# Kernel optimization log

Measured on AMD Instinct MI355X. Metric: run time of the kernel, lower is better.

## Reference

```python
import jax, jax.numpy as jnp
import numpy as np

B, T, J = 64, 1024, 22
PARENTS = [0, 0, 1, 2, 3, 0, 5, 6, 7, 0, 9, 10, 11, 12, 11, 14, 15, 16, 11, 18, 19, 20]
SPARSE_JOINTS = [0, 4, 8, 13, 17, 21]
EE = tuple(SPARSE_JOINTS[1:])                       # end effectors (sparse_joints[1:])
NO_SPARSE = tuple(j for j in range(J) if j not in SPARSE_JOINTS)
LAMBDA_EE, LAMBDA_EE_REG = 1.0, 0.1
IDENT_DQ = np.array([1, 0, 0, 0, 0, 0, 0, 0], dtype=np.float32)


def _qconj(q):
    return q * jnp.array([1.0, -1.0, -1.0, -1.0], q.dtype)


def _qmul(a, b):
    aw, ax, ay, az = a[..., 0], a[..., 1], a[..., 2], a[..., 3]
    bw, bx, by, bz = b[..., 0], b[..., 1], b[..., 2], b[..., 3]
    return jnp.stack([
        aw * bw - ax * bx - ay * by - az * bz,
        aw * bx + ax * bw + ay * bz - az * by,
        aw * by - ax * bz + ay * bw + az * bx,
        aw * bz + ax * by - ay * bx + az * bw], axis=-1)


def _qrot(q, v):
    # rotate vector v by unit quaternion q
    qv = q[..., 1:]
    t = 2.0 * jnp.cross(qv, v)
    return v + q[..., :1] * t + jnp.cross(qv, t)


def _qmat(q):
    w, x, y, z = q[..., 0], q[..., 1], q[..., 2], q[..., 3]
    m = jnp.stack([
        1 - 2 * (y * y + z * z), 2 * (x * y - w * z), 2 * (x * z + w * y),
        2 * (x * y + w * z), 1 - 2 * (x * x + z * z), 2 * (y * z - w * x),
        2 * (x * z - w * y), 2 * (y * z + w * x), 1 - 2 * (x * x + y * y)], axis=-1)
    return m.reshape(m.shape[:-1] + (3, 3))


def _denorm_to_dq(x, mean, std, set_root_identity):
    # x: (B, J*8, T) channel-major dual quats -> (B, T, J, 8)
    x = x * std[None, :, None] + mean[None, :, None]
    if set_root_identity:
        x = x.at[:, :8, :].set(jnp.asarray(IDENT_DQ, x.dtype)[None, :, None])
    b, c, t = x.shape
    return x.reshape(b, c // 8, 8, t).transpose(0, 3, 1, 2)


def _local_rot_from_dq(dq):
    # skeleton_from_dual_quat: real part = global rotation; make local via parent gather
    qr = dq[..., :4]
    qr = qr / jnp.linalg.norm(qr, axis=-1, keepdims=True)
    parent = jnp.asarray(PARENTS)
    local = _qmul(_qconj(qr[:, :, parent, :]), qr)   # (B,T,J,4)
    # forward_ik overwrites root local rotation with identity
    local = local.at[:, :, 0, :].set(jnp.array([1.0, 0.0, 0.0, 0.0], dq.dtype))
    return local


def _fk(local_rot, offsets):
    # fk_2: sequential parent-indexed propagation; root global pos is zeros
    rots = [local_rot[:, :, 0]]
    poss = [jnp.zeros(local_rot.shape[:2] + (3,), local_rot.dtype)]
    for j in range(1, J):
        p = PARENTS[j]
        rots.append(_qmul(rots[p], local_rot[:, :, j]))
        poss.append(_qrot(rots[p], offsets[j]) + poss[p])
    grot = jnp.stack(rots, axis=2)          # (B,T,J,4)
    pos = jnp.stack(poss, axis=2)           # (B,T,J,3)
    return pos, _qmat(grot)                  # positions, (B,T,J,3,3) rot matrices


def setup_inputs() -> dict:
    key = jax.random.key(0)
    ks = jax.random.split(key, 7)
    C = J * 8
    return {
        "input": jax.random.normal(ks[0], (B, C, T), jnp.float32),
        "input_ik": jax.random.normal(ks[1], (B, C - 8, T), jnp.float32),
        "input_decoder": jax.random.normal(ks[2], (B, C, T), jnp.float32),
        "target": jax.random.normal(ks[3], (B, C, T), jnp.float32),
        "mean_dqs": 0.1 * jax.random.normal(ks[4], (C,), jnp.float32),
        "std_dqs": 0.5 + 0.5 * jax.random.uniform(ks[5], (C,), jnp.float32),
        "offsets": jax.random.normal(ks[6], (J, 3), jnp.float32),
    }


def reference(input, input_ik, input_decoder, target, mean_dqs, std_dqs, offsets):
    # prepend identity-slot for the root (8 zero channels), then denormalize
    dq_ik = jnp.concatenate([jnp.zeros_like(input_ik[:, :8, :]), input_ik], axis=1)
    dq_ik = _denorm_to_dq(dq_ik, mean_dqs, std_dqs, True)
    dq_dec = _denorm_to_dq(input_decoder, mean_dqs, std_dqs, True)
    dq_tgt = _denorm_to_dq(target, mean_dqs, std_dqs, False)

    r_ik = _local_rot_from_dq(dq_ik)
    r_dec = _local_rot_from_dq(dq_dec)
    r_tgt = _local_rot_from_dq(dq_tgt)

    pos, rm = _fk(r_ik, offsets)
    tpos, trm = _fk(r_tgt, offsets)
    dpos, drm = _fk(r_dec, offsets)

    ee = jnp.asarray(EE)
    ns = jnp.asarray(NO_SPARSE)
    mse = lambda a, b: jnp.mean((a - b) ** 2)
    loss_ee = mse(pos[:, :, ee], tpos[:, :, ee]) + mse(rm[:, :, ee], trm[:, :, ee])
    loss_reg = mse(dpos[:, :, ns], pos[:, :, ns]) + mse(drm[:, :, ns], rm[:, :, ns])
    return loss_ee * LAMBDA_EE + loss_reg * LAMBDA_EE_REG
```

## Files before the change

kernel.cpp:

```cpp
#include <hip/hip_runtime.h>


#define T_DIM 1024

struct Q { float w, x, y, z; };
struct V3 { float x, y, z; };
struct St { Q rot; V3 pos; };

__device__ __forceinline__ Q qmul(const Q a, const Q b) {
    Q r;
    r.w = a.w*b.w - a.x*b.x - a.y*b.y - a.z*b.z;
    r.x = a.w*b.x + a.x*b.w + a.y*b.z - a.z*b.y;
    r.y = a.w*b.y - a.x*b.z + a.y*b.w + a.z*b.x;
    r.z = a.w*b.z + a.x*b.y - a.y*b.x + a.z*b.w;
    return r;
}

__device__ __forceinline__ V3 qrot(const Q q, const V3 v) {
    float tx = 2.f*(q.y*v.z - q.z*v.y);
    float ty = 2.f*(q.z*v.x - q.x*v.z);
    float tz = 2.f*(q.x*v.y - q.y*v.x);
    V3 r;
    r.x = v.x + q.w*tx + (q.y*tz - q.z*ty);
    r.y = v.y + q.w*ty + (q.z*tx - q.x*tz);
    r.z = v.z + q.w*tz + (q.x*ty - q.y*tx);
    return r;
}

__device__ __forceinline__ float rmdiff2u(const Q a, const Q b) {
    float d = a.w*b.w + a.x*b.x + a.y*b.y + a.z*b.z;
    return 8.f*(1.f - d*d);
}

__device__ __forceinline__ float pdiff2(const V3 a, const V3 b) {
    float dx=a.x-b.x, dy=a.y-b.y, dz=a.z-b.z;
    return dx*dx+dy*dy+dz*dz;
}

__device__ __forceinline__ V3 v3add(const V3 a, const V3 b) {
    return V3{a.x+b.x, a.y+b.y, a.z+b.z};
}

__device__ __forceinline__ Q mkq(const float r[4], const int c0,
                                 const float* __restrict__ mean,
                                 const float* __restrict__ stdv) {
    Q q;
    q.w = r[0]*stdv[c0+0] + mean[c0+0];
    q.x = r[1]*stdv[c0+1] + mean[c0+1];
    q.y = r[2]*stdv[c0+2] + mean[c0+2];
    q.z = r[3]*stdv[c0+3] + mean[c0+3];
    float inv = rsqrtf(q.w*q.w + q.x*q.x + q.y*q.y + q.z*q.z);
    q.w*=inv; q.x*=inv; q.y*=inv; q.z*=inv;
    return q;
}

template<int J0, int N>
__device__ __forceinline__ void pf2(
    const float* __restrict__ xp, const float* __restrict__ yp,
    float (*xr)[4], float (*yr)[4])
{
#pragma unroll
    for (int jj = 0; jj < N; ++jj) {
        const int j = J0 + jj;
#pragma unroll
        for (int c = 0; c < 4; ++c) {
            xr[jj][c] = xp[(j*8 + c)*T_DIM];
            yr[jj][c] = yp[(j*8 + c)*T_DIM];
        }
    }
}

template<int J, bool LOSS, bool PRE>
__device__ __forceinline__ void step2(
    St& sx, St& sy,
    const float xr[4], const float yr[4],
    const float* __restrict__ mean, const float* __restrict__ stdv,
    const float* __restrict__ offs, const Q q0c,
    float& ap, float& ar)
{
    const int c0 = J*8;
    Q qx = mkq(xr, c0, mean, stdv);
    Q qy = mkq(yr, c0, mean, stdv);
    if (PRE) qy = qmul(q0c, qy);
    V3 off = { offs[3*J], offs[3*J+1], offs[3*J+2] };
    V3 px = v3add(qrot(sx.rot, off), sx.pos);
    V3 py = v3add(qrot(sy.rot, off), sy.pos);
    if (LOSS) {
        ap += pdiff2(px, py);
        ar += rmdiff2u(qx, qy);
    }
    sx.rot = qx; sx.pos = px;
    sy.rot = qy; sy.pos = py;
}

template<bool EEROLE>
__device__ __forceinline__ void walk(
    const float* __restrict__ xp, const float* __restrict__ yp,
    const float* __restrict__ mean, const float* __restrict__ stdv,
    const float* __restrict__ offs,
    float& ap, float& ar)
{
    float Xa[4][4], Ya[4][4];
    float Xb[4][4], Yb[4][4];
    float Xc[5][4], Yc[5][4];
    float Xd[4][4], Yd[4][4];
    float Xe[4][4], Ye[4][4];
    float rq0[4];

    if (EEROLE) {
#pragma unroll
        for (int c = 0; c < 4; ++c) rq0[c] = yp[c*T_DIM];
    }
    pf2<1,4>(xp, yp, Xa, Ya);
    pf2<5,4>(xp, yp, Xb, Yb);

    Q q0c = {1.f, 0.f, 0.f, 0.f};
    if (EEROLE) {
        Q q0 = mkq(rq0, 0, mean, stdv);
        q0c = { q0.w, -q0.x, -q0.y, -q0.z };
    }
    const St root = { {1.f,0.f,0.f,0.f}, {0.f,0.f,0.f} };
    St sx, sy;

    sx = root; sy = root;
    step2<1, !EEROLE, EEROLE>(sx,sy, Xa[0],Ya[0], mean,stdv,offs,q0c, ap,ar);
    step2<2, !EEROLE, EEROLE>(sx,sy, Xa[1],Ya[1], mean,stdv,offs,q0c, ap,ar);
    step2<3, !EEROLE, EEROLE>(sx,sy, Xa[2],Ya[2], mean,stdv,offs,q0c, ap,ar);
    step2<4,  EEROLE, EEROLE>(sx,sy, Xa[3],Ya[3], mean,stdv,offs,q0c, ap,ar);

    pf2<9,5>(xp, yp, Xc, Yc);

    sx = root; sy = root;
    step2<5, !EEROLE, EEROLE>(sx,sy, Xb[0],Yb[0], mean,stdv,offs,q0c, ap,ar);
    step2<6, !EEROLE, EEROLE>(sx,sy, Xb[1],Yb[1], mean,stdv,offs,q0c, ap,ar);
    step2<7, !EEROLE, EEROLE>(sx,sy, Xb[2],Yb[2], mean,stdv,offs,q0c, ap,ar);
    step2<8,  EEROLE, EEROLE>(sx,sy, Xb[3],Yb[3], mean,stdv,offs,q0c, ap,ar);

    pf2<14,4>(xp, yp, Xd, Yd);

    sx = root; sy = root;
    step2<9,  !EEROLE, EEROLE>(sx,sy, Xc[0],Yc[0], mean,stdv,offs,q0c, ap,ar);
    step2<10, !EEROLE, EEROLE>(sx,sy, Xc[1],Yc[1], mean,stdv,offs,q0c, ap,ar);
    step2<11, !EEROLE, EEROLE>(sx,sy, Xc[2],Yc[2], mean,stdv,offs,q0c, ap,ar);
    const St sx11 = sx, sy11 = sy;
    step2<12, !EEROLE, EEROLE>(sx,sy, Xc[3],Yc[3], mean,stdv,offs,q0c, ap,ar);
    step2<13,  EEROLE, EEROLE>(sx,sy, Xc[4],Yc[4], mean,stdv,offs,q0c, ap,ar);

    pf2<18,4>(xp, yp, Xe, Ye);

    sx = sx11; sy = sy11;
    step2<14, !EEROLE, EEROLE>(sx,sy, Xd[0],Yd[0], mean,stdv,offs,q0c, ap,ar);
    step2<15, !EEROLE, EEROLE>(sx,sy, Xd[1],Yd[1], mean,stdv,offs,q0c, ap,ar);
    step2<16, !EEROLE, EEROLE>(sx,sy, Xd[2],Yd[2], mean,stdv,offs,q0c, ap,ar);
    step2<17,  EEROLE, EEROLE>(sx,sy, Xd[3],Yd[3], mean,stdv,offs,q0c, ap,ar);

    sx = sx11; sy = sy11;
    step2<18, !EEROLE, EEROLE>(sx,sy, Xe[0],Ye[0], mean,stdv,offs,q0c, ap,ar);
    step2<19, !EEROLE, EEROLE>(sx,sy, Xe[1],Ye[1], mean,stdv,offs,q0c, ap,ar);
    step2<20, !EEROLE, EEROLE>(sx,sy, Xe[2],Ye[2], mean,stdv,offs,q0c, ap,ar);
    step2<21,  EEROLE, EEROLE>(sx,sy, Xe[3],Ye[3], mean,stdv,offs,q0c, ap,ar);
}

__global__ __launch_bounds__(256, 2) void fk_loss_kernel(
    const float* __restrict__ ik, const float* __restrict__ dec,
    const float* __restrict__ tgt, const float* __restrict__ mean,
    const float* __restrict__ stdv, const float* __restrict__ offs,
    float* __restrict__ out)
{
    __shared__ float swred[4];
    const int tid = threadIdx.x;
    const int bid = blockIdx.x;
    const int role = bid >> 8;
    const int pose_blk = bid & 255;

    const int p = pose_blk * 256 + tid;
    const int b = p >> 10;
    const int t = p & 1023;
    const float* ikp = ik  + (size_t)b * (168*1024) + t - (size_t)(8*T_DIM);
    const float* dep = dec + (size_t)b * (176*1024) + t;
    const float* tgp = tgt + (size_t)b * (176*1024) + t;

    float ap = 0.f, ar = 0.f;
    float loss;
    const float BT = 65536.f;
    if (role == 0) {
        walk<true>(ikp, tgp, mean, stdv, offs, ap, ar);
        loss = ap * (1.0f/(BT*15.f)) + ar * (1.0f/(BT*45.f));
    } else {
        walk<false>(dep, ikp, mean, stdv, offs, ap, ar);
        loss = ap * (0.1f/(BT*48.f)) + ar * (0.1f/(BT*144.f));
    }

#pragma unroll
    for (int o = 32; o > 0; o >>= 1) loss += __shfl_down(loss, o);
    if ((tid & 63) == 0) swred[tid >> 6] = loss;
    __syncthreads();
    if (tid == 0) {
        atomicAdd(out, swred[0]+swred[1]+swred[2]+swred[3]);
    }
}

extern "C" void kernel_launch(void* const* d_in, const int* in_sizes, int n_in,
                              void* d_out, int out_size, void* d_ws, size_t ws_size,
                              hipStream_t stream) {
    const float* ikx  = (const float*)d_in[1];
    const float* dec  = (const float*)d_in[2];
    const float* tgt  = (const float*)d_in[3];
    const float* mean = (const float*)d_in[4];
    const float* stdv = (const float*)d_in[5];
    const float* offs = (const float*)d_in[6];
    float* out = (float*)d_out;

    hipMemsetAsync(out, 0, sizeof(float), stream);
    fk_loss_kernel<<<512, 256, 0, stream>>>(ikx, dec, tgt, mean, stdv, offs, out);
}
```

Before: 195.4 us.

## Process two timesteps per thread with float2 loads and packed math

Each thread now handles two adjacent timesteps using 8-byte float2 loads and paired arithmetic that can map to packed FP32 instructions. The grid is halved to 256 blocks. The prefetch plan changes from deep whole-chain register buffers to a smaller reused buffer loaded in pieces, and the occupancy hint in launch bounds is dropped. This aims to improve load width and ALU throughput, but it halves the number of threads, which lowers latency hiding for a memory-bound kernel and leaves most CUs partly idle.

```diff
diff --git a/kernel.cpp b/kernel.cpp
--- a/kernel.cpp
+++ b/kernel.cpp
@@ -3,12 +3,23 @@
 
 #define T_DIM 1024
 
-struct Q { float w, x, y, z; };
-struct V3 { float x, y, z; };
-struct St { Q rot; V3 pos; };
-
-__device__ __forceinline__ Q qmul(const Q a, const Q b) {
-    Q r;
+struct alignas(8) F2 { float u, v; };
+
+__device__ __forceinline__ F2 operator+(F2 a, F2 b){ return {a.u+b.u, a.v+b.v}; }
+__device__ __forceinline__ F2 operator-(F2 a, F2 b){ return {a.u-b.u, a.v-b.v}; }
+__device__ __forceinline__ F2 operator*(F2 a, F2 b){ return {a.u*b.u, a.v*b.v}; }
+__device__ __forceinline__ F2 operator*(F2 a, float s){ return {a.u*s, a.v*s}; }
+__device__ __forceinline__ F2 operator+(F2 a, float s){ return {a.u+s, a.v+s}; }
+__device__ __forceinline__ F2 f2neg(F2 a){ return {-a.u, -a.v}; }
+__device__ __forceinline__ F2 f2bc(float s){ return {s, s}; }
+__device__ __forceinline__ F2 f2rsq(F2 a){ return {rsqrtf(a.u), rsqrtf(a.v)}; }
+
+struct Q2 { F2 w, x, y, z; };
+struct V2 { F2 x, y, z; };
+struct St2 { Q2 rot; V2 pos; };
+
+__device__ __forceinline__ Q2 qmul2(const Q2 a, const Q2 b) {
+    Q2 r;
     r.w = a.w*b.w - a.x*b.x - a.y*b.y - a.z*b.z;
     r.x = a.w*b.x + a.x*b.w + a.y*b.z - a.z*b.y;
     r.y = a.w*b.y - a.x*b.z + a.y*b.w + a.z*b.x;
@@ -16,78 +27,79 @@
     return r;
 }
 
-__device__ __forceinline__ V3 qrot(const Q q, const V3 v) {
-    float tx = 2.f*(q.y*v.z - q.z*v.y);
-    float ty = 2.f*(q.z*v.x - q.x*v.z);
-    float tz = 2.f*(q.x*v.y - q.y*v.x);
-    V3 r;
-    r.x = v.x + q.w*tx + (q.y*tz - q.z*ty);
-    r.y = v.y + q.w*ty + (q.z*tx - q.x*tz);
-    r.z = v.z + q.w*tz + (q.x*ty - q.y*tx);
+__device__ __forceinline__ V2 qrot2(const Q2 q, float ox, float oy, float oz) {
+    F2 tx = (q.y*oz - q.z*oy)*2.f;
+    F2 ty = (q.z*ox - q.x*oz)*2.f;
+    F2 tz = (q.x*oy - q.y*ox)*2.f;
+    V2 r;
+    r.x = (q.w*tx + (q.y*tz - q.z*ty)) + ox;
+    r.y = (q.w*ty + (q.z*tx - q.x*tz)) + oy;
+    r.z = (q.w*tz + (q.x*ty - q.y*tx)) + oz;
     return r;
 }
 
-__device__ __forceinline__ float rmdiff2u(const Q a, const Q b) {
-    float d = a.w*b.w + a.x*b.x + a.y*b.y + a.z*b.z;
-    return 8.f*(1.f - d*d);
-}
-
-__device__ __forceinline__ float pdiff2(const V3 a, const V3 b) {
-    float dx=a.x-b.x, dy=a.y-b.y, dz=a.z-b.z;
-    return dx*dx+dy*dy+dz*dz;
-}
-
-__device__ __forceinline__ V3 v3add(const V3 a, const V3 b) {
-    return V3{a.x+b.x, a.y+b.y, a.z+b.z};
-}
-
-__device__ __forceinline__ Q mkq(const float r[4], const int c0,
-                                 const float* __restrict__ mean,
-                                 const float* __restrict__ stdv) {
-    Q q;
+__device__ __forceinline__ F2 rmdiff2u(const Q2 a, const Q2 b) {
+    F2 d = a.w*b.w + a.x*b.x + a.y*b.y + a.z*b.z;
+    return (f2bc(1.f) - d*d)*8.f;
+}
+
+__device__ __forceinline__ F2 pdiff2(const V2 a, const V2 b) {
+    F2 dx = a.x-b.x, dy = a.y-b.y, dz = a.z-b.z;
+    return dx*dx + dy*dy + dz*dz;
+}
+
+__device__ __forceinline__ Q2 mkq2(const F2 r[4], const int c0,
+                                   const float* __restrict__ mean,
+                                   const float* __restrict__ stdv) {
+    Q2 q;
     q.w = r[0]*stdv[c0+0] + mean[c0+0];
     q.x = r[1]*stdv[c0+1] + mean[c0+1];
     q.y = r[2]*stdv[c0+2] + mean[c0+2];
     q.z = r[3]*stdv[c0+3] + mean[c0+3];
-    float inv = rsqrtf(q.w*q.w + q.x*q.x + q.y*q.y + q.z*q.z);
-    q.w*=inv; q.x*=inv; q.y*=inv; q.z*=inv;
+    F2 inv = f2rsq(q.w*q.w + q.x*q.x + q.y*q.y + q.z*q.z);
+    q.w = q.w*inv; q.x = q.x*inv; q.y = q.y*inv; q.z = q.z*inv;
     return q;
 }
 
+__device__ __forceinline__ F2 ld2(const float* __restrict__ base, int idx) {
+    return *reinterpret_cast<const F2*>(base + idx);
+}
+
 template<int J0, int N>
-__device__ __forceinline__ void pf2(
-    const float* __restrict__ xp, const float* __restrict__ yp,
-    float (*xr)[4], float (*yr)[4])
+__device__ __forceinline__ void ldb(
+    const float* __restrict__ xp, const float* __restrict__ yp, const int t0,
+    F2 (*X)[4], F2 (*Y)[4])
 {
 #pragma unroll
     for (int jj = 0; jj < N; ++jj) {
-        const int j = J0 + jj;
 #pragma unroll
         for (int c = 0; c < 4; ++c) {
-            xr[jj][c] = xp[(j*8 + c)*T_DIM];
-            yr[jj][c] = yp[(j*8 + c)*T_DIM];
+            X[jj][c] = ld2(xp, ((J0+jj)*8 + c)*T_DIM + t0);
+            Y[jj][c] = ld2(yp, ((J0+jj)*8 + c)*T_DIM + t0);
         }
     }
 }
 
 template<int J, bool LOSS, bool PRE>
-__device__ __forceinline__ void step2(
-    St& sx, St& sy,
-    const float xr[4], const float yr[4],
+__device__ __forceinline__ void stepf(
+    St2& sx, St2& sy,
+    const F2 xr[4], const F2 yr[4],
     const float* __restrict__ mean, const float* __restrict__ stdv,
-    const float* __restrict__ offs, const Q q0c,
-    float& ap, float& ar)
+    const float* __restrict__ offs, const Q2& q0c,
+    F2& ap, F2& ar)
 {
     const int c0 = J*8;
-    Q qx = mkq(xr, c0, mean, stdv);
-    Q qy = mkq(yr, c0, mean, stdv);
-    if (PRE) qy = qmul(q0c, qy);
-    V3 off = { offs[3*J], offs[3*J+1], offs[3*J+2] };
-    V3 px = v3add(qrot(sx.rot, off), sx.pos);
-    V3 py = v3add(qrot(sy.rot, off), sy.pos);
+    Q2 qx = mkq2(xr, c0, mean, stdv);
+    Q2 qy = mkq2(yr, c0, mean, stdv);
+    if (PRE) qy = qmul2(q0c, qy);
+    const float ox = offs[3*J], oy = offs[3*J+1], oz = offs[3*J+2];
+    V2 dx = qrot2(sx.rot, ox, oy, oz);
+    V2 dy = qrot2(sy.rot, ox, oy, oz);
+    V2 px = { dx.x + sx.pos.x, dx.y + sx.pos.y, dx.z + sx.pos.z };
+    V2 py = { dy.x + sy.pos.x, dy.y + sy.pos.y, dy.z + sy.pos.z };
     if (LOSS) {
-        ap += pdiff2(px, py);
-        ar += rmdiff2u(qx, qy);
+        ap = ap + pdiff2(px, py);
+        ar = ar + rmdiff2u(qx, qy);
     }
     sx.rot = qx; sx.pos = px;
     sy.rot = qy; sy.pos = py;
@@ -95,73 +107,69 @@
 
 template<bool EEROLE>
 __device__ __forceinline__ void walk(
-    const float* __restrict__ xp, const float* __restrict__ yp,
+    const float* __restrict__ xp, const float* __restrict__ yp, const int t0,
     const float* __restrict__ mean, const float* __restrict__ stdv,
-    const float* __restrict__ offs,
-    float& ap, float& ar)
-{
-    float Xa[4][4], Ya[4][4];
-    float Xb[4][4], Yb[4][4];
-    float Xc[5][4], Yc[5][4];
-    float Xd[4][4], Yd[4][4];
-    float Xe[4][4], Ye[4][4];
-    float rq0[4];
+    const float* __restrict__ offs, F2& ap, F2& ar)
+{
+    F2 X[4][4], Y[4][4];
+    F2 rq0[4];
 
     if (EEROLE) {
 #pragma unroll
-        for (int c = 0; c < 4; ++c) rq0[c] = yp[c*T_DIM];
-    }
-    pf2<1,4>(xp, yp, Xa, Ya);
-    pf2<5,4>(xp, yp, Xb, Yb);
-
-    Q q0c = {1.f, 0.f, 0.f, 0.f};
+        for (int c = 0; c < 4; ++c) rq0[c] = ld2(yp, c*T_DIM + t0);
+    }
+    ldb<1,4>(xp, yp, t0, X, Y);
+
+    Q2 q0c = { f2bc(1.f), f2bc(0.f), f2bc(0.f), f2bc(0.f) };
     if (EEROLE) {
-        Q q0 = mkq(rq0, 0, mean, stdv);
-        q0c = { q0.w, -q0.x, -q0.y, -q0.z };
-    }
-    const St root = { {1.f,0.f,0.f,0.f}, {0.f,0.f,0.f} };
-    St sx, sy;
+        Q2 q0 = mkq2(rq0, 0, mean, stdv);
+        q0c = { q0.w, f2neg(q0.x), f2neg(q0.y), f2neg(q0.z) };
+    }
+    const St2 root = { { f2bc(1.f), f2bc(0.f), f2bc(0.f), f2bc(0.f) },
+                       { f2bc(0.f), f2bc(0.f), f2bc(0.f) } };
+    St2 sx, sy;
 
     sx = root; sy = root;
-    step2<1, !EEROLE, EEROLE>(sx,sy, Xa[0],Ya[0], mean,stdv,offs,q0c, ap,ar);
-    step2<2, !EEROLE, EEROLE>(sx,sy, Xa[1],Ya[1], mean,stdv,offs,q0c, ap,ar);
-    step2<3, !EEROLE, EEROLE>(sx,sy, Xa[2],Ya[2], mean,stdv,offs,q0c, ap,ar);
-    step2<4,  EEROLE, EEROLE>(sx,sy, Xa[3],Ya[3], mean,stdv,offs,q0c, ap,ar);
-
-    pf2<9,5>(xp, yp, Xc, Yc);
-
+    stepf<1, !EEROLE, EEROLE>(sx,sy, X[0],Y[0], mean,stdv,offs,q0c, ap,ar);
+    stepf<2, !EEROLE, EEROLE>(sx,sy, X[1],Y[1], mean,stdv,offs,q0c, ap,ar);
+    stepf<3, !EEROLE, EEROLE>(sx,sy, X[2],Y[2], mean,stdv,offs,q0c, ap,ar);
+    stepf<4,  EEROLE, EEROLE>(sx,sy, X[3],Y[3], mean,stdv,offs,q0c, ap,ar);
+
+    ldb<5,4>(xp, yp, t0, X, Y);
     sx = root; sy = root;
-    step2<5, !EEROLE, EEROLE>(sx,sy, Xb[0],Yb[0], mean,stdv,offs,q0c, ap,ar);
-    step2<6, !EEROLE, EEROLE>(sx,sy, Xb[1],Yb[1], mean,stdv,offs,q0c, ap,ar);
-    step2<7, !EEROLE, EEROLE>(sx,sy, Xb[2],Yb[2], mean,stdv,offs,q0c, ap,ar);
-    step2<8,  EEROLE, EEROLE>(sx,sy, Xb[3],Yb[3], mean,stdv,offs,q0c, ap,ar);
-
-    pf2<14,4>(xp, yp, Xd, Yd);
-
+    stepf<5, !EEROLE, EEROLE>(sx,sy, X[0],Y[0], mean,stdv,offs,q0c, ap,ar);
+    stepf<6, !EEROLE, EEROLE>(sx,sy, X[1],Y[1], mean,stdv,offs,q0c, ap,ar);
+    stepf<7, !EEROLE, EEROLE>(sx,sy, X[2],Y[2], mean,stdv,offs,q0c, ap,ar);
+    stepf<8,  EEROLE, EEROLE>(sx,sy, X[3],Y[3], mean,stdv,offs,q0c, ap,ar);
+
+    ldb<9,3>(xp, yp, t0, X, Y);
     sx = root; sy = root;
-    step2<9,  !EEROLE, EEROLE>(sx,sy, Xc[0],Yc[0], mean,stdv,offs,q0c, ap,ar);
-    step2<10, !EEROLE, EEROLE>(sx,sy, Xc[1],Yc[1], mean,stdv,offs,q0c, ap,ar);
-    step2<11, !EEROLE, EEROLE>(sx,sy, Xc[2],Yc[2], mean,stdv,offs,q0c, ap,ar);
-    const St sx11 = sx, sy11 = sy;
-    step2<12, !EEROLE, EEROLE>(sx,sy, Xc[3],Yc[3], mean,stdv,offs,q0c, ap,ar);
-    step2<13,  EEROLE, EEROLE>(sx,sy, Xc[4],Yc[4], mean,stdv,offs,q0c, ap,ar);
-
-    pf2<18,4>(xp, yp, Xe, Ye);
-
+    stepf<9,  !EEROLE, EEROLE>(sx,sy, X[0],Y[0], mean,stdv,offs,q0c, ap,ar);
+    stepf<10, !EEROLE, EEROLE>(sx,sy, X[1],Y[1], mean,stdv,offs,q0c, ap,ar);
+    stepf<11, !EEROLE, EEROLE>(sx,sy, X[2],Y[2], mean,stdv,offs,q0c, ap,ar);
+    const St2 sx11 = sx, sy11 = sy;
+    ldb<12,2>(xp, yp, t0, X, Y);
+    stepf<12, !EEROLE, EEROLE>(sx,sy, X[0],Y[0], mean,stdv,offs,q0c, ap,ar);
+    stepf<13,  EEROLE, EEROLE>(sx,sy, X[1],Y[1], mean,stdv,offs,q0c, ap,ar);
+
+    ldb<14,2>(xp, yp, t0, X, Y);
     sx = sx11; sy = sy11;
-    step2<14, !EEROLE, EEROLE>(sx,sy, Xd[0],Yd[0], mean,stdv,offs,q0c, ap,ar);
-    step2<15, !EEROLE, EEROLE>(sx,sy, Xd[1],Yd[1], mean,stdv,offs,q0c, ap,ar);
-    step2<16, !EEROLE, EEROLE>(sx,sy, Xd[2],Yd[2], mean,stdv,offs,q0c, ap,ar);
-    step2<17,  EEROLE, EEROLE>(sx,sy, Xd[3],Yd[3], mean,stdv,offs,q0c, ap,ar);
-
+    stepf<14, !EEROLE, EEROLE>(sx,sy, X[0],Y[0], mean,stdv,offs,q0c, ap,ar);
+    stepf<15, !EEROLE, EEROLE>(sx,sy, X[1],Y[1], mean,stdv,offs,q0c, ap,ar);
+    ldb<16,2>(xp, yp, t0, X, Y);
+    stepf<16, !EEROLE, EEROLE>(sx,sy, X[0],Y[0], mean,stdv,offs,q0c, ap,ar);
+    stepf<17,  EEROLE, EEROLE>(sx,sy, X[1],Y[1], mean,stdv,offs,q0c, ap,ar);
+
+    ldb<18,2>(xp, yp, t0, X, Y);
     sx = sx11; sy = sy11;
-    step2<18, !EEROLE, EEROLE>(sx,sy, Xe[0],Ye[0], mean,stdv,offs,q0c, ap,ar);
-    step2<19, !EEROLE, EEROLE>(sx,sy, Xe[1],Ye[1], mean,stdv,offs,q0c, ap,ar);
-    step2<20, !EEROLE, EEROLE>(sx,sy, Xe[2],Ye[2], mean,stdv,offs,q0c, ap,ar);
-    step2<21,  EEROLE, EEROLE>(sx,sy, Xe[3],Ye[3], mean,stdv,offs,q0c, ap,ar);
-}
-
-__global__ __launch_bounds__(256, 2) void fk_loss_kernel(
+    stepf<18, !EEROLE, EEROLE>(sx,sy, X[0],Y[0], mean,stdv,offs,q0c, ap,ar);
+    stepf<19, !EEROLE, EEROLE>(sx,sy, X[1],Y[1], mean,stdv,offs,q0c, ap,ar);
+    ldb<20,2>(xp, yp, t0, X, Y);
+    stepf<20, !EEROLE, EEROLE>(sx,sy, X[0],Y[0], mean,stdv,offs,q0c, ap,ar);
+    stepf<21,  EEROLE, EEROLE>(sx,sy, X[1],Y[1], mean,stdv,offs,q0c, ap,ar);
+}
+
+__global__ __launch_bounds__(256) void fk_loss_kernel(
     const float* __restrict__ ik, const float* __restrict__ dec,
     const float* __restrict__ tgt, const float* __restrict__ mean,
     const float* __restrict__ stdv, const float* __restrict__ offs,
@@ -170,25 +178,26 @@
     __shared__ float swred[4];
     const int tid = threadIdx.x;
     const int bid = blockIdx.x;
-    const int role = bid >> 8;
-    const int pose_blk = bid & 255;
-
-    const int p = pose_blk * 256 + tid;
-    const int b = p >> 10;
-    const int t = p & 1023;
-    const float* ikp = ik  + (size_t)b * (168*1024) + t - (size_t)(8*T_DIM);
-    const float* dep = dec + (size_t)b * (176*1024) + t;
-    const float* tgp = tgt + (size_t)b * (176*1024) + t;
-
-    float ap = 0.f, ar = 0.f;
+    const int role = bid >> 7;
+    const int pb   = bid & 127;
+    const int bb   = pb >> 1;
+    const int t0   = (pb & 1)*512 + 2*tid;
+
+    const float* ikp = ik  + (size_t)bb * (168*1024) - (size_t)(8*T_DIM);
+    const float* dep = dec + (size_t)bb * (176*1024);
+    const float* tgp = tgt + (size_t)bb * (176*1024);
+
+    F2 ap = f2bc(0.f), ar = f2bc(0.f);
     float loss;
     const float BT = 65536.f;
     if (role == 0) {
-        walk<true>(ikp, tgp, mean, stdv, offs, ap, ar);
-        loss = ap * (1.0f/(BT*15.f)) + ar * (1.0f/(BT*45.f));
+        walk<true>(ikp, tgp, t0, mean, stdv, offs, ap, ar);
+        loss = (ap.u + ap.v) * (1.0f/(BT*15.f))
+             + (ar.u + ar.v) * (1.0f/(BT*45.f));
     } else {
-        walk<false>(dep, ikp, mean, stdv, offs, ap, ar);
-        loss = ap * (0.1f/(BT*48.f)) + ar * (0.1f/(BT*144.f));
+        walk<false>(dep, ikp, t0, mean, stdv, offs, ap, ar);
+        loss = (ap.u + ap.v) * (0.1f/(BT*48.f))
+             + (ar.u + ar.v) * (0.1f/(BT*144.f));
     }
 
 #pragma unroll
@@ -212,5 +221,5 @@
     float* out = (float*)d_out;
 
     hipMemsetAsync(out, 0, sizeof(float), stream);
-    fk_loss_kernel<<<512, 256, 0, stream>>>(ikx, dec, tgt, mean, stdv, offs, out);
-}
+    fk_loss_kernel<<<256, 256, 0, stream>>>(ikx, dec, tgt, mean, stdv, offs, out);
+}
```

Measured after the change: 181.9 us. 6.9% less time.
